# Kernel tuning notes

Measured on AMD Instinct MI355X. Metric: run time of the kernel, lower is better.

The kernel has to match this reference:

```python
import jax, jax.numpy as jnp
import numpy as np

B, C, IMG, P = 8, 6, 384, 16
DIM, HEADS, DEPTH, MLP, NCLS = 768, 12, 4, 3072, 1000
N = (IMG // P) ** 2            # 576 patches
DH = DIM // HEADS              # 64
PATCH_DIM = C * P * P          # 1536


def setup_inputs() -> dict:
    key = jax.random.key(0)
    ks = jax.random.split(key, 13)
    f = lambda k, shp, s=0.02: jax.random.normal(k, shp, jnp.float32) * s
    return {
        "x": jax.random.normal(ks[0], (B, C, IMG, IMG), jnp.float32),
        "patch_w": f(ks[1], (PATCH_DIM, DIM)),
        "patch_b": f(ks[2], (DIM,)),
        "ln1_g": jnp.ones((DEPTH, DIM), jnp.float32),
        "ln1_b": jnp.zeros((DEPTH, DIM), jnp.float32),
        "w_qkv": f(ks[3], (DEPTH, DIM, 3 * DIM)),
        "bias_att": f(ks[4], (DEPTH, HEADS, N, N), 0.5),
        "w_out": f(ks[5], (DEPTH, DIM, DIM)),
        "ln2_g": jnp.ones((DEPTH, DIM), jnp.float32),
        "ln2_b": jnp.zeros((DEPTH, DIM), jnp.float32),
        "w1": f(ks[6], (DEPTH, DIM, MLP)),
        "b1": f(ks[7], (DEPTH, MLP)),
        "w2": f(ks[8], (DEPTH, MLP, DIM)),
        "b2": f(ks[9], (DEPTH, DIM)),
        "lnh_g": jnp.ones((DIM,), jnp.float32),
        "lnh_b": jnp.zeros((DIM,), jnp.float32),
        "w_head": f(ks[10], (DIM, NCLS)),
        "b_head": f(ks[11], (NCLS,)),
    }


def _ln(x, g, b, eps=1e-5):
    m = x.mean(-1, keepdims=True)
    v = ((x - m) ** 2).mean(-1, keepdims=True)
    return (x - m) * jax.lax.rsqrt(v + eps) * g + b


def _patchify(x, patch_w, patch_b):
    # Rearrange 'b c (h p1) (w p2) -> b (h w) (p1 p2 c)' then Linear(patch_dim, dim)
    b = x.shape[0]
    g = IMG // P
    x = x.reshape(b, C, g, P, g, P).transpose(0, 2, 4, 3, 5, 1).reshape(b, g * g, PATCH_DIM)
    return x @ patch_w + patch_b


def _forward(x, patch_w, patch_b, ln1_g, ln1_b, w_qkv, bias_att, w_out,
             ln2_g, ln2_b, w1, b1, w2, b2, lnh_g, lnh_b, w_head, b_head):
    scale = DH ** -0.5
    tok = _patchify(x, patch_w, patch_b)  # [B, N, DIM]; pos_info='mul_att_normed' -> no pos_embed added

    def block(t, p):
        l1g, l1b, wqkv, bias, wout, l2g, l2b, ww1, bb1, ww2, bb2 = p
        h = _ln(t, l1g, l1b)
        qkv = h @ wqkv                                     # [B, N, 3*DIM]
        q, k, v = jnp.split(qkv, 3, axis=-1)
        rs = lambda a: a.reshape(t.shape[0], N, HEADS, DH).transpose(0, 2, 1, 3)
        q, k, v = rs(q), rs(k), rs(v)                      # [B, H, N, DH]
        dots = jnp.einsum('bhid,bhjd->bhij', q, k) * scale
        # mul_att_normed: softmax(qk) * softmax(bias), renormalized over keys
        attn = jax.nn.softmax(dots, axis=-1) * jax.nn.softmax(bias, axis=-1)[None]
        attn = attn / attn.sum(-1, keepdims=True)
        o = jnp.einsum('bhij,bhjd->bhid', attn, v)
        o = o.transpose(0, 2, 1, 3).reshape(t.shape[0], N, DIM) @ wout
        t = t + o
        h2 = _ln(t, l2g, l2b)
        t = t + (jax.nn.gelu(h2 @ ww1 + bb1, approximate=False) @ ww2 + bb2)
        return t, None

    tok, _ = jax.lax.scan(block, tok,
                          (ln1_g, ln1_b, w_qkv, bias_att, w_out,
                           ln2_g, ln2_b, w1, b1, w2, b2))
    pooled = tok.mean(axis=1)                              # mean-pool tokens
    return _ln(pooled, lnh_g, lnh_b) @ w_head + b_head     # [B, NCLS]


def reference(x, patch_w, patch_b, ln1_g, ln1_b, w_qkv, bias_att, w_out,
              ln2_g, ln2_b, w1, b1, w2, b2, lnh_g, lnh_b, w_head, b_head):
    return _forward(x, patch_w, patch_b, ln1_g, ln1_b, w_qkv, bias_att, w_out,
                    ln2_g, ln2_b, w1, b1, w2, b2, lnh_g, lnh_b, w_head, b_head)
```

## Files before the change

kernel.cpp:

```cpp
#include <hip/hip_runtime.h>
#include <hip/hip_bf16.h>

typedef __attribute__((ext_vector_type(8))) short bf16x8;
typedef __attribute__((ext_vector_type(4))) float f32x4;

#define DEVI __device__ __forceinline__

DEVI unsigned short f2bf_bits(float f) {
    __hip_bfloat16 h = __float2bfloat16(f);
    return *reinterpret_cast<unsigned short*>(&h);
}
DEVI float bfbits2f(unsigned short u) {
    __hip_bfloat16 h = *reinterpret_cast<__hip_bfloat16*>(&u);
    return __bfloat162float(h);
}

DEVI void gload_lds16(const void* g, void* lds) {
    __builtin_amdgcn_global_load_lds(
        (const __attribute__((address_space(1))) unsigned int*)g,
        (__attribute__((address_space(3))) unsigned int*)lds, 16, 0, 0);
}

template <int N> DEVI void wait_vm() {
    if constexpr (N == 0) asm volatile("s_waitcnt vmcnt(0)" ::: "memory");
    else if constexpr (N == 4) asm volatile("s_waitcnt vmcnt(4)" ::: "memory");
    else if constexpr (N == 6) asm volatile("s_waitcnt vmcnt(6)" ::: "memory");
    else if constexpr (N == 12) asm volatile("s_waitcnt vmcnt(12)" ::: "memory");
    __builtin_amdgcn_sched_barrier(0);
}
DEVI void lgkm0() {
    asm volatile("s_waitcnt lgkmcnt(0)" ::: "memory");
    __builtin_amdgcn_sched_barrier(0);
}

DEVI int2 remap2d(int bid, int total, int gx) {
    int q = total >> 3, r = total & 7, x = bid & 7, l = bid >> 3;
    int seq = (x < r ? x * (q + 1) : r * (q + 1) + (x - r) * q) + l;
    int g4 = seq / (4 * gx);
    int rem = seq - g4 * 4 * gx;
    return {g4 * 4 + (rem & 3), rem >> 2};
}
DEVI int2 remap2d_g2(int bid, int total, int gx) {
    int q = total >> 3, r = total & 7, x = bid & 7, l = bid >> 3;
    int seq = (x < r ? x * (q + 1) : r * (q + 1) + (x - r) * q) + l;
    int g2 = seq / (2 * gx);
    int rem = seq - g2 * 2 * gx;
    return {g2 * 2 + (rem & 1), rem >> 1};
}

__global__ __launch_bounds__(256) void patchify_kernel(const float* __restrict__ x,
                                                       unsigned short* __restrict__ patches)
{
    size_t t8 = (size_t)blockIdx.x * 256 + threadIdx.x;
    int jq = (int)(t8 % 48);
    size_t t = t8 / 48;
    int r = (int)(t % 384); t /= 384;
    int c = (int)(t % 6);
    int b = (int)(t / 6);
    int j = jq * 8;
    int gh = r >> 4, p1 = r & 15, gw = j >> 4, p2 = j & 15;
    int prow = b * 576 + gh * 24 + gw;
    int pcol = c * 256 + p1 * 16 + p2;
    const float* src = x + ((((size_t)b * 6 + c) * 384 + r) * 384 + j);
    float4 v0 = ((const float4*)src)[0];
    float4 v1 = ((const float4*)src)[1];
    ushort u[8] = { f2bf_bits(v0.x), f2bf_bits(v0.y), f2bf_bits(v0.z), f2bf_bits(v0.w),
                    f2bf_bits(v1.x), f2bf_bits(v1.y), f2bf_bits(v1.z), f2bf_bits(v1.w) };
    *(int4*)&patches[(size_t)prow * 1536 + pcol] = *(int4*)u;
}

__global__ __launch_bounds__(256) void convT_patch_kernel(const float* __restrict__ W,
                                                          __hip_bfloat16* __restrict__ Wt)
{
    __shared__ float tile[32][33];
    int n0 = blockIdx.x * 32, kp0 = blockIdx.y * 32;
    int tx = threadIdx.x & 31, ty = threadIdx.x >> 5;
#pragma unroll
    for (int i = 0; i < 4; i++) {
        int kp = kp0 + ty + 8 * i;
        int k = (kp & 255) * 6 + (kp >> 8);
        tile[ty + 8 * i][tx] = W[(size_t)k * 768 + n0 + tx];
    }
    __syncthreads();
#pragma unroll
    for (int i = 0; i < 4; i++)
        Wt[(size_t)(n0 + ty + 8 * i) * 1536 + kp0 + tx] = __float2bfloat16(tile[tx][ty + 8 * i]);
}

DEVI void convT_body(const float* __restrict__ W, __hip_bfloat16* __restrict__ Wt,
                     int K, int N, int k0, int n0, int tid)
{
    __shared__ float tile[32][33];
    int tx = tid & 31, ty = tid >> 5;
#pragma unroll
    for (int i = 0; i < 4; i++)
        tile[ty + 8 * i][tx] = W[(size_t)(k0 + ty + 8 * i) * N + n0 + tx];
    __syncthreads();
#pragma unroll
    for (int i = 0; i < 4; i++)
        Wt[(size_t)(n0 + ty + 8 * i) * K + k0 + tx] = __float2bfloat16(tile[tx][ty + 8 * i]);
}

__global__ __launch_bounds__(256) void convT4_kernel(const float* __restrict__ wqkv,
                                                     const float* __restrict__ wout,
                                                     const float* __restrict__ w1,
                                                     const float* __restrict__ w2,
                                                     __hip_bfloat16* __restrict__ dst)
{
    int bt = blockIdx.x;
    const float* W; __hip_bfloat16* Wt; int K, N, lt;
    if (bt < 1728)      { W = wqkv; K = 768;  N = 2304; lt = bt;        Wt = dst; }
    else if (bt < 2304) { W = wout; K = 768;  N = 768;  lt = bt - 1728; Wt = dst + 1769472; }
    else if (bt < 4608) { W = w1;   K = 768;  N = 3072; lt = bt - 2304; Wt = dst + 2359296; }
    else                { W = w2;   K = 3072; N = 768;  lt = bt - 4608; Wt = dst + 4718592; }
    int tn = N >> 5;
    convT_body(W, Wt, K, N, (lt / tn) * 32, (lt % tn) * 32, threadIdx.x);
}

DEVI float ld_ln(const float* p) { return *p; }
DEVI float ld_ln(const __hip_bfloat16* p) { return __bfloat162float(*p); }
DEVI void st_ln(float* p, float v) { *p = v; }
DEVI void st_ln(__hip_bfloat16* p, float v) { *p = __float2bfloat16(v); }

template <typename InT, typename OutT>
__global__ __launch_bounds__(256) void ln_kernel(const InT* __restrict__ x,
                                                 const float* __restrict__ g,
                                                 const float* __restrict__ b,
                                                 OutT* __restrict__ out)
{
    int row = blockIdx.x, tid = threadIdx.x;
    const InT* xr = x + (size_t)row * 768;
    float v0 = ld_ln(&xr[tid]), v1 = ld_ln(&xr[tid + 256]), v2 = ld_ln(&xr[tid + 512]);
    float s = v0 + v1 + v2;
    float s2 = v0 * v0 + v1 * v1 + v2 * v2;
#pragma unroll
    for (int m = 32; m >= 1; m >>= 1) { s += __shfl_xor(s, m); s2 += __shfl_xor(s2, m); }
    __shared__ float red[8];
    int w = tid >> 6;
    if ((tid & 63) == 0) { red[w] = s; red[4 + w] = s2; }
    __syncthreads();
    s = red[0] + red[1] + red[2] + red[3];
    s2 = red[4] + red[5] + red[6] + red[7];
    float mean = s * (1.0f / 768.0f);
    float var = s2 * (1.0f / 768.0f) - mean * mean;
    float rstd = rsqrtf(var + 1e-5f);
    OutT* orow = out + (size_t)row * 768;
    st_ln(&orow[tid], (v0 - mean) * rstd * g[tid] + b[tid]);
    st_ln(&orow[tid + 256], (v1 - mean) * rstd * g[tid + 256] + b[tid + 256]);
    st_ln(&orow[tid + 512], (v2 - mean) * rstd * g[tid + 512] + b[tid + 512]);
}

template <bool BIAS, bool GELU>
__global__ __launch_bounds__(512, 2) void gemm_8ph_kernel(
    const __hip_bfloat16* __restrict__ A,
    const __hip_bfloat16* __restrict__ Bt,
    const float* __restrict__ bias,
    __hip_bfloat16* __restrict__ Cb,
    int M, int N, int K, int gx)
{
    __shared__ __align__(16) __hip_bfloat16 AsF[32768];
    __shared__ __align__(16) __hip_bfloat16 BsF[32768];
    const int tid = threadIdx.x;
    const int wid = tid >> 6, lane = tid & 63;
    const int g = lane >> 4, l16 = lane & 15;
    const int wmh = wid >> 2, wnn = wid & 3;

    int2 bc = remap2d_g2(blockIdx.x, gridDim.x, gx);
    const int bm = bc.x * 256, bn = bc.y * 256;

    const int srow = tid >> 2;
    size_t aS[2], bS[2];
#pragma unroll
    for (int i = 0; i < 2; i++) {
        int row = i * 128 + srow;
        int lc = (tid & 3) ^ ((row >> 1) & 3);
        aS[i] = (size_t)(bm + row) * K + lc * 8;
        bS[i] = (size_t)(bn + row) * K + lc * 8;
    }
    auto stageA = [&](int buf, int kh, int tq) {
        const __hip_bfloat16* ap = A + (size_t)tq * 64 + kh * 32;
        __hip_bfloat16* dst = AsF + (buf * 2 + kh) * 8192;
        gload_lds16(ap + aS[0], dst + tid * 8);
        gload_lds16(ap + aS[1], dst + 4096 + tid * 8);
    };
    auto stageB = [&](int buf, int kh, int tq) {
        const __hip_bfloat16* bp = Bt + (size_t)tq * 64 + kh * 32;
        __hip_bfloat16* dst = BsF + (buf * 2 + kh) * 8192;
        gload_lds16(bp + bS[0], dst + tid * 8);
        gload_lds16(bp + bS[1], dst + 4096 + tid * 8);
    };

    const int csw = (l16 >> 1) & 3;
    const int rdo = (g ^ csw) << 3;
    const int aBase = (wmh * 128 + l16) * 32 + rdo;
    const int bBase = (wnn * 64 + l16) * 32 + rdo;

    f32x4 acc[8][4] = {};
    const int nt = K >> 6;

    stageA(0, 0, 0); stageB(0, 0, 0); stageA(0, 1, 0); stageB(0, 1, 0);
    stageA(1, 0, 1); stageB(1, 0, 1);
    wait_vm<4>();
    __builtin_amdgcn_s_barrier();
    __builtin_amdgcn_sched_barrier(0);

    bf16x8 af[8], bf2[2];
    for (int t = 0; t < nt; t++) {
        const int b = t & 1;
        const int k0 = (b * 2 + 0) * 8192, k1 = (b * 2 + 1) * 8192;

#pragma unroll
        for (int mi = 0; mi < 8; mi++) af[mi] = *(const bf16x8*)&AsF[k0 + aBase + mi * 512];
        bf2[0] = *(const bf16x8*)&BsF[k0 + bBase + 0 * 512];
        bf2[1] = *(const bf16x8*)&BsF[k0 + bBase + 1 * 512];
        if (t + 1 < nt) stageA(b ^ 1, 1, t + 1);
        __builtin_amdgcn_s_barrier(); lgkm0();
        __builtin_amdgcn_s_setprio(1);
#pragma unroll
        for (int mi = 0; mi < 8; mi++) {
            acc[mi][0] = __builtin_amdgcn_mfma_f32_16x16x32_bf16(af[mi], bf2[0], acc[mi][0], 0, 0, 0);
            acc[mi][1] = __builtin_amdgcn_mfma_f32_16x16x32_bf16(af[mi], bf2[1], acc[mi][1], 0, 0, 0);
        }
        __builtin_amdgcn_s_setprio(0);
        __builtin_amdgcn_s_barrier();

        bf2[0] = *(const bf16x8*)&BsF[k0 + bBase + 2 * 512];
        bf2[1] = *(const bf16x8*)&BsF[k0 + bBase + 3 * 512];
        if (t + 1 < nt) stageB(b ^ 1, 1, t + 1);
        __builtin_amdgcn_s_barrier(); lgkm0();
        __builtin_amdgcn_s_setprio(1);
#pragma unroll
        for (int mi = 0; mi < 8; mi++) {
            acc[mi][2] = __builtin_amdgcn_mfma_f32_16x16x32_bf16(af[mi], bf2[0], acc[mi][2], 0, 0, 0);
            acc[mi][3] = __builtin_amdgcn_mfma_f32_16x16x32_bf16(af[mi], bf2[1], acc[mi][3], 0, 0, 0);
        }
        __builtin_amdgcn_s_setprio(0);
        __builtin_amdgcn_s_barrier();

#pragma unroll
        for (int mi = 0; mi < 8; mi++) af[mi] = *(const bf16x8*)&AsF[k1 + aBase + mi * 512];
        bf2[0] = *(const bf16x8*)&BsF[k1 + bBase + 0 * 512];
        bf2[1] = *(const bf16x8*)&BsF[k1 + bBase + 1 * 512];
        if (t + 2 < nt) stageA(b, 0, t + 2);
        __builtin_amdgcn_s_barrier(); lgkm0();
        __builtin_amdgcn_s_setprio(1);
#pragma unroll
        for (int mi = 0; mi < 8; mi++) {
            acc[mi][0] = __builtin_amdgcn_mfma_f32_16x16x32_bf16(af[mi], bf2[0], acc[mi][0], 0, 0, 0);
            acc[mi][1] = __builtin_amdgcn_mfma_f32_16x16x32_bf16(af[mi], bf2[1], acc[mi][1], 0, 0, 0);
        }
        __builtin_amdgcn_s_setprio(0);
        __builtin_amdgcn_s_barrier();

        bf2[0] = *(const bf16x8*)&BsF[k1 + bBase + 2 * 512];
        bf2[1] = *(const bf16x8*)&BsF[k1 + bBase + 3 * 512];
        if (t + 2 < nt) stageB(b, 0, t + 2);
        __builtin_amdgcn_s_barrier(); lgkm0();
        __builtin_amdgcn_s_setprio(1);
#pragma unroll
        for (int mi = 0; mi < 8; mi++) {
            acc[mi][2] = __builtin_amdgcn_mfma_f32_16x16x32_bf16(af[mi], bf2[0], acc[mi][2], 0, 0, 0);
            acc[mi][3] = __builtin_amdgcn_mfma_f32_16x16x32_bf16(af[mi], bf2[1], acc[mi][3], 0, 0, 0);
        }
        __builtin_amdgcn_s_setprio(0);
        if (t + 2 < nt) wait_vm<4>();
        else            wait_vm<0>();
        __builtin_amdgcn_s_barrier();
        __builtin_amdgcn_sched_barrier(0);
    }

    __hip_bfloat16* scr = AsF + wid * (16 * 72);
#pragma unroll
    for (int mi = 0; mi < 8; mi++) {
#pragma unroll
        for (int ni = 0; ni < 4; ni++) {
            float bval = 0.0f;
            if (BIAS) bval = bias[bn + wnn * 64 + ni * 16 + l16];
#pragma unroll
            for (int r = 0; r < 4; r++) {
                float v = acc[mi][ni][r] + bval;
                if (GELU) v = 0.5f * v * (1.0f + erff(v * 0.70710678118654752f));
                scr[(4 * g + r) * 72 + ni * 16 + l16] = __float2bfloat16(v);
            }
        }
        lgkm0();
#pragma unroll
        for (int q2 = 0; q2 < 2; q2++) {
            int idx = q2 * 64 + lane;
            int row16 = idx >> 3, ch = idx & 7;
            bf16x8 vv = *(const bf16x8*)&scr[row16 * 72 + ch * 8];
            int grow = bm + wmh * 128 + mi * 16 + row16;
            *(int4*)&Cb[(size_t)grow * N + bn + wnn * 64 + ch * 8] = *(int4*)&vv;
        }
        lgkm0();
    }
}

template <bool BIAS, bool RESID>
__global__ __launch_bounds__(256, 2) void gemm_bt_kernel(
    const __hip_bfloat16* __restrict__ A,
    const __hip_bfloat16* __restrict__ Bt,
    const float* __restrict__ bias,
    const __hip_bfloat16* __restrict__ resid,
    __hip_bfloat16* __restrict__ Cb,
    int M, int N, int K, int gx)
{
    constexpr int BM = 64, SL = 6;
    __shared__ __align__(16) __hip_bfloat16 As[3][BM * 64];
    __shared__ __align__(16) __hip_bfloat16 Bs[3][128 * 64];
    const int tid = threadIdx.x;
    const int wid = tid >> 6, lane = tid & 63;
    const int g = lane >> 4, l16 = lane & 15;
    const int wm = (wid >> 1) * 32, wn = (wid & 1) * 64;

    int2 bc = remap2d(blockIdx.x, gridDim.x, gx);
    const int bm = bc.x * BM, bn = bc.y * 128;

    const int sr32 = tid >> 3, ci = tid & 7;
    const int cg = ci ^ (sr32 & 7);
    const int sdst = tid * 8;
    size_t aOff[2], bOff[4];
#pragma unroll
    for (int i = 0; i < 2; i++) aOff[i] = (size_t)(bm + i * 32 + sr32) * K + cg * 8;
#pragma unroll
    for (int i = 0; i < 4; i++) bOff[i] = (size_t)(bn + i * 32 + sr32) * K + cg * 8;

    auto stage = [&](__hip_bfloat16* asb, __hip_bfloat16* bsb, int tq) {
        const __hip_bfloat16* ap = A + tq * 64;
        const __hip_bfloat16* bp = Bt + tq * 64;
#pragma unroll
        for (int i = 0; i < 2; i++) gload_lds16(ap + aOff[i], asb + i * 2048 + sdst);
#pragma unroll
        for (int i = 0; i < 4; i++) gload_lds16(bp + bOff[i], bsb + i * 2048 + sdst);
    };

    f32x4 acc[2][4] = {};
    const int nt = K >> 6;

    stage(As[0], Bs[0], 0);
    stage(As[1], Bs[1], 1);
    stage(As[2], Bs[2], 2);
    wait_vm<12>();
    __builtin_amdgcn_s_barrier();
    __builtin_amdgcn_sched_barrier(0);

    for (int t = 0; t < nt; t += 3) {
#pragma unroll
        for (int u = 0; u < 3; u++) {
            const int tc = t + u;
            bf16x8 af[2][2], bfr[2][4];
#pragma unroll
            for (int s = 0; s < 2; s++) {
                const int cp = ((s * 4 + g) ^ (l16 & 7)) << 3;
#pragma unroll
                for (int mi = 0; mi < 2; mi++)
                    af[s][mi] = *(const bf16x8*)&As[u][(wm + mi * 16 + l16) * 64 + cp];
#pragma unroll
                for (int ni = 0; ni < 4; ni++)
                    bfr[s][ni] = *(const bf16x8*)&Bs[u][(wn + ni * 16 + l16) * 64 + cp];
            }
#pragma unroll
            for (int s = 0; s < 2; s++)
#pragma unroll
                for (int mi = 0; mi < 2; mi++)
#pragma unroll
                    for (int ni = 0; ni < 4; ni++)
                        acc[mi][ni] = __builtin_amdgcn_mfma_f32_16x16x32_bf16(af[s][mi], bfr[s][ni], acc[mi][ni], 0, 0, 0);

            lgkm0();
            __builtin_amdgcn_s_barrier();
            __builtin_amdgcn_sched_barrier(0);

            if (tc + 3 < nt) stage(As[u], Bs[u], tc + 3);
            if (tc + 1 < nt) {
                if (tc + 4 <= nt)      wait_vm<12>();
                else if (tc + 3 == nt) wait_vm<6>();
                else                   wait_vm<0>();
                __builtin_amdgcn_s_barrier();
                __builtin_amdgcn_sched_barrier(0);
            }
        }
    }

    __hip_bfloat16* scr = &As[0][0] + wid * (16 * 72);
#pragma unroll
    for (int mi = 0; mi < 2; mi++) {
#pragma unroll
        for (int ni = 0; ni < 4; ni++) {
            float bval = 0.0f;
            if (BIAS) bval = bias[bn + wn + ni * 16 + l16];
#pragma unroll
            for (int r = 0; r < 4; r++)
                scr[(4 * g + r) * 72 + ni * 16 + l16] = __float2bfloat16(acc[mi][ni][r] + bval);
        }
        lgkm0();
#pragma unroll
        for (int q2 = 0; q2 < 2; q2++) {
            int row16 = q2 * 8 + (lane >> 3), ch = lane & 7;
            bf16x8 vv = *(const bf16x8*)&scr[row16 * 72 + ch * 8];
            int grow = bm + wm + mi * 16 + row16;
            size_t off = (size_t)grow * N + bn + wn + ch * 8;
            if (RESID) {
                bf16x8 rv = *(const bf16x8*)&resid[off];
#pragma unroll
                for (int e = 0; e < 8; e++)
                    vv[e] = (short)f2bf_bits(bfbits2f((unsigned short)vv[e]) + bfbits2f((unsigned short)rv[e]));
            }
            *(int4*)&Cb[off] = *(int4*)&vv;
        }
        lgkm0();
    }
}

__global__ __launch_bounds__(256) void attn_kernel(const __hip_bfloat16* __restrict__ qkvb,
                                                   const float* __restrict__ bias,
                                                   unsigned short* __restrict__ o)
{
    const int seq = (blockIdx.x & 7) * 108 + (blockIdx.x >> 3);
    const int bb = seq & 7, qt = (seq >> 3) % 9, h = seq / 72;
    const int q0 = qt * 64;
    const int tid = threadIdx.x;
    const int wq = tid >> 6, lane = tid & 63, g = lane >> 4, l16 = lane & 15;

    __shared__ __align__(16) unsigned short Qs[64 * 72];
    __shared__ __align__(16) unsigned short Ks[64 * 72];
    __shared__ __align__(16) unsigned short Vt[64 * 72];
    __shared__ __align__(16) unsigned short Ps[4][16 * 72];

    {
        int r = tid >> 2, cb = (tid & 3) * 16;
        const int4* s4 = (const int4*)&qkvb[(size_t)(bb * 576 + q0 + r) * 2304 + h * 64 + cb];
        int4* d4 = (int4*)&Qs[r * 72 + cb];
        d4[0] = s4[0]; d4[1] = s4[1];
    }
    __syncthreads();
    bf16x8 qf0 = *(const bf16x8*)&Qs[(wq * 16 + l16) * 72 + g * 8];
    bf16x8 qf1 = *(const bf16x8*)&Qs[(wq * 16 + l16) * 72 + 32 + g * 8];

    float m_r[4] = {-1e30f, -1e30f, -1e30f, -1e30f};
    float l_r[4] = {0.f, 0.f, 0.f, 0.f};
    f32x4 oa[4] = {};
    const float* bias_h = bias + (size_t)h * 576 * 576;
    const float scale = 0.125f;

    for (int kt = 0; kt < 576; kt += 64) {
        {
            int r = tid >> 2, cb = (tid & 3) * 16;
            const int4* s4 = (const int4*)&qkvb[(size_t)(bb * 576 + kt + r) * 2304 + 768 + h * 64 + cb];
            int4* d4 = (int4*)&Ks[r * 72 + cb];
            d4[0] = s4[0]; d4[1] = s4[1];
            int key = tid & 63, d0 = (tid >> 6) * 16;
            const unsigned short* vs = (const unsigned short*)&qkvb[(size_t)(bb * 576 + kt + key) * 2304 + 1536 + h * 64 + d0];
            bf16x8 v0 = *(const bf16x8*)vs;
            bf16x8 v1 = *(const bf16x8*)(vs + 8);
#pragma unroll
            for (int e = 0; e < 8; e++) {
                Vt[(d0 + e) * 72 + key] = (unsigned short)v0[e];
                Vt[(d0 + 8 + e) * 72 + key] = (unsigned short)v1[e];
            }
        }
        __syncthreads();

        float bl[4][4];
#pragma unroll
        for (int kc = 0; kc < 4; kc++)
#pragma unroll
            for (int r = 0; r < 4; r++) {
                int q = q0 + wq * 16 + 4 * g + r;
                bl[kc][r] = bias_h[(size_t)q * 576 + kt + kc * 16 + l16];
            }

        f32x4 sc[4] = {};
        __builtin_amdgcn_s_setprio(1);
#pragma unroll
        for (int kc = 0; kc < 4; kc++) {
            bf16x8 kf0 = *(const bf16x8*)&Ks[(kc * 16 + l16) * 72 + g * 8];
            bf16x8 kf1 = *(const bf16x8*)&Ks[(kc * 16 + l16) * 72 + 32 + g * 8];
            sc[kc] = __builtin_amdgcn_mfma_f32_16x16x32_bf16(qf0, kf0, sc[kc], 0, 0, 0);
            sc[kc] = __builtin_amdgcn_mfma_f32_16x16x32_bf16(qf1, kf1, sc[kc], 0, 0, 0);
        }
        __builtin_amdgcn_s_setprio(0);

        float sv[4][4], mt[4] = {-1e30f, -1e30f, -1e30f, -1e30f};
#pragma unroll
        for (int kc = 0; kc < 4; kc++)
#pragma unroll
            for (int r = 0; r < 4; r++) {
                float s = sc[kc][r] * scale + bl[kc][r];
                sv[kc][r] = s;
                mt[r] = fmaxf(mt[r], s);
            }
#pragma unroll
        for (int r = 0; r < 4; r++)
#pragma unroll
            for (int m = 1; m < 16; m <<= 1) mt[r] = fmaxf(mt[r], __shfl_xor(mt[r], m));

        float sf[4];
#pragma unroll
        for (int r = 0; r < 4; r++) {
            float mn = fmaxf(m_r[r], mt[r]);
            sf[r] = __expf(m_r[r] - mn);
            m_r[r] = mn;
        }
        float rs[4] = {0.f, 0.f, 0.f, 0.f};
#pragma unroll
        for (int kc = 0; kc < 4; kc++)
#pragma unroll
            for (int r = 0; r < 4; r++) {
                float p = __expf(sv[kc][r] - m_r[r]);
                rs[r] += p;
                Ps[wq][(4 * g + r) * 72 + kc * 16 + l16] = f2bf_bits(p);
            }
#pragma unroll
        for (int r = 0; r < 4; r++) {
#pragma unroll
            for (int m = 1; m < 16; m <<= 1) rs[r] += __shfl_xor(rs[r], m);
            l_r[r] = l_r[r] * sf[r] + rs[r];
        }
#pragma unroll
        for (int dt = 0; dt < 4; dt++)
#pragma unroll
            for (int r = 0; r < 4; r++) oa[dt][r] *= sf[r];

        asm volatile("s_waitcnt lgkmcnt(0)" ::: "memory");

        __builtin_amdgcn_s_setprio(1);
#pragma unroll
        for (int s = 0; s < 2; s++) {
            bf16x8 pf = *(const bf16x8*)&Ps[wq][l16 * 72 + s * 32 + g * 8];
#pragma unroll
            for (int dt = 0; dt < 4; dt++) {
                bf16x8 vf = *(const bf16x8*)&Vt[(dt * 16 + l16) * 72 + s * 32 + g * 8];
                oa[dt] = __builtin_amdgcn_mfma_f32_16x16x32_bf16(pf, vf, oa[dt], 0, 0, 0);
            }
        }
        __builtin_amdgcn_s_setprio(0);
        __syncthreads();
    }

#pragma unroll
    for (int dt = 0; dt < 4; dt++)
#pragma unroll
        for (int r = 0; r < 4; r++) {
            int q = q0 + wq * 16 + 4 * g + r;
            float v = oa[dt][r] / l_r[r];
            o[(size_t)(bb * 576 + q) * 768 + h * 64 + dt * 16 + l16] = f2bf_bits(v);
        }
}

__global__ __launch_bounds__(256) void pool_kernel(const __hip_bfloat16* __restrict__ tok,
                                                   float* __restrict__ pooled)
{
    int d = blockIdx.x * 256 + threadIdx.x;
    int b = blockIdx.y;
    float s = 0.0f;
    for (int n = 0; n < 576; n++) s += __bfloat162float(tok[(size_t)(b * 576 + n) * 768 + d]);
    pooled[b * 768 + d] = s * (1.0f / 576.0f);
}

__global__ __launch_bounds__(256) void head_kernel(const float* __restrict__ lnp,
                                                   const float* __restrict__ w,
                                                   const float* __restrict__ bh,
                                                   float* __restrict__ out)
{
    int c = blockIdx.x * 256 + threadIdx.x;
    int b = blockIdx.y;
    if (c >= 1000) return;
    float s = bh[c];
    for (int d = 0; d < 768; d++) s += lnp[b * 768 + d] * w[(size_t)d * 1000 + c];
    out[b * 1000 + c] = s;
}

extern "C" void kernel_launch(void* const* d_in, const int* in_sizes, int n_in,
                              void* d_out, int out_size, void* d_ws, size_t ws_size,
                              hipStream_t stream)
{
    const float* x = (const float*)d_in[0];
    const float* patch_w = (const float*)d_in[1];
    const float* patch_b = (const float*)d_in[2];
    const float* ln1_g = (const float*)d_in[3];
    const float* ln1_b = (const float*)d_in[4];
    const float* w_qkv = (const float*)d_in[5];
    const float* bias_att = (const float*)d_in[6];
    const float* w_out = (const float*)d_in[7];
    const float* ln2_g = (const float*)d_in[8];
    const float* ln2_b = (const float*)d_in[9];
    const float* w1 = (const float*)d_in[10];
    const float* b1 = (const float*)d_in[11];
    const float* w2 = (const float*)d_in[12];
    const float* b2 = (const float*)d_in[13];
    const float* lnh_g = (const float*)d_in[14];
    const float* lnh_b = (const float*)d_in[15];
    const float* w_head = (const float*)d_in[16];
    const float* b_head = (const float*)d_in[17];
    float* out = (float*)d_out;

    char* ws = (char*)d_ws;
    __hip_bfloat16* tok = (__hip_bfloat16*)(ws + 0);
    __hip_bfloat16* qkv_bf = (__hip_bfloat16*)(ws + 14155776);
    float* pooled = (float*)(ws + 56623104);
    float* pooledln = (float*)(ws + 56647680);
    __hip_bfloat16* patches = (__hip_bfloat16*)(ws + 56672256);
    __hip_bfloat16* lw = patches;
    __hip_bfloat16* h_bf = (__hip_bfloat16*)(ws + 70828032);
    __hip_bfloat16* o_bf = (__hip_bfloat16*)(ws + 77905920);
    __hip_bfloat16* hid_bf = (__hip_bfloat16*)(ws + 84983808);
    __hip_bfloat16* wbuf = (__hip_bfloat16*)(ws + 113295360);

    patchify_kernel<<<3456, 256, 0, stream>>>(x, (unsigned short*)patches);
    convT_patch_kernel<<<dim3(24, 48), 256, 0, stream>>>(patch_w, wbuf);
    gemm_bt_kernel<true, false><<<432, 256, 0, stream>>>(
        patches, wbuf, patch_b, nullptr, tok, 4608, 768, 1536, 6);

    for (int l = 0; l < 4; l++) {
        convT4_kernel<<<6912, 256, 0, stream>>>(
            w_qkv + (size_t)l * 768 * 2304, w_out + (size_t)l * 768 * 768,
            w1 + (size_t)l * 768 * 3072, w2 + (size_t)l * 3072 * 768, lw);
        ln_kernel<__hip_bfloat16, __hip_bfloat16><<<4608, 256, 0, stream>>>(
            tok, ln1_g + l * 768, ln1_b + l * 768, h_bf);
        gemm_8ph_kernel<false, false><<<162, 512, 0, stream>>>(
            h_bf, lw, nullptr, qkv_bf, 4608, 2304, 768, 9);
        attn_kernel<<<864, 256, 0, stream>>>(
            qkv_bf, bias_att + (size_t)l * 12 * 576 * 576, (unsigned short*)o_bf);
        gemm_bt_kernel<false, true><<<432, 256, 0, stream>>>(
            o_bf, lw + 1769472, nullptr, tok, tok, 4608, 768, 768, 6);
        ln_kernel<__hip_bfloat16, __hip_bfloat16><<<4608, 256, 0, stream>>>(
            tok, ln2_g + l * 768, ln2_b + l * 768, h_bf);
        gemm_8ph_kernel<true, true><<<216, 512, 0, stream>>>(
            h_bf, lw + 2359296, b1 + l * 3072, hid_bf, 4608, 3072, 768, 12);
        gemm_bt_kernel<true, true><<<432, 256, 0, stream>>>(
            hid_bf, lw + 4718592, b2 + l * 768, tok, tok, 4608, 768, 3072, 6);
    }

    pool_kernel<<<dim3(3, 8), 256, 0, stream>>>(tok, pooled);
    ln_kernel<float, float><<<8, 256, 0, stream>>>(pooled, lnh_g, lnh_b, pooledln);
    head_kernel<<<dim3(4, 8), 256, 0, stream>>>(pooledln, w_head, b_head, out);
}
```

Before: 835.7 us.

## Fold LayerNorm into GEMM epilogues via precomputed weight coefficients and row stats

LayerNorm is removed as a separate pass. The gamma scale is folded into the transposed bf16 weights, and per-column sums of beta·W and gamma·W are precomputed. A light stats kernel computes per-row mean and rstd, and the QKV and MLP1 GEMMs apply the normalization in their epilogue while reading the raw token tensor directly. When the workspace is large enough, the weight conversion for all layers runs in one launch before the layer loop. This cuts the h_bf write/read traffic and the per-layer launches, at the cost of numerical differences: the GEMM now runs on unnormalized bf16 tokens with a mean-subtraction correction, and lncoef uses a serial 768-long loop per thread.

```diff
diff --git a/kernel.cpp b/kernel.cpp
--- a/kernel.cpp
+++ b/kernel.cpp
@@ -88,6 +88,7 @@
 }
 
 DEVI void convT_body(const float* __restrict__ W, __hip_bfloat16* __restrict__ Wt,
+                     const float* __restrict__ gvec,
                      int K, int N, int k0, int n0, int tid)
 {
     __shared__ float tile[32][33];
@@ -96,65 +97,138 @@
     for (int i = 0; i < 4; i++)
         tile[ty + 8 * i][tx] = W[(size_t)(k0 + ty + 8 * i) * N + n0 + tx];
     __syncthreads();
+    float gk = gvec ? gvec[k0 + tx] : 1.0f;
 #pragma unroll
     for (int i = 0; i < 4; i++)
-        Wt[(size_t)(n0 + ty + 8 * i) * K + k0 + tx] = __float2bfloat16(tile[tx][ty + 8 * i]);
+        Wt[(size_t)(n0 + ty + 8 * i) * K + k0 + tx] = __float2bfloat16(tile[tx][ty + 8 * i] * gk);
+}
+
+DEVI void convT4_dispatch(int bt, const float* wqkv, const float* wout,
+                          const float* w1, const float* w2,
+                          const float* g1, const float* g2,
+                          __hip_bfloat16* dst, int tid)
+{
+    const float* W; const float* gv = nullptr; __hip_bfloat16* Wt; int K, N, lt;
+    if (bt < 1728)      { W = wqkv; K = 768;  N = 2304; lt = bt;        Wt = dst;           gv = g1; }
+    else if (bt < 2304) { W = wout; K = 768;  N = 768;  lt = bt - 1728; Wt = dst + 1769472; }
+    else if (bt < 4608) { W = w1;   K = 768;  N = 3072; lt = bt - 2304; Wt = dst + 2359296; gv = g2; }
+    else                { W = w2;   K = 3072; N = 768;  lt = bt - 4608; Wt = dst + 4718592; }
+    int tn = N >> 5;
+    convT_body(W, Wt, gv, K, N, (lt / tn) * 32, (lt % tn) * 32, tid);
 }
 
 __global__ __launch_bounds__(256) void convT4_kernel(const float* __restrict__ wqkv,
                                                      const float* __restrict__ wout,
                                                      const float* __restrict__ w1,
                                                      const float* __restrict__ w2,
+                                                     const float* __restrict__ g1,
+                                                     const float* __restrict__ g2,
                                                      __hip_bfloat16* __restrict__ dst)
 {
-    int bt = blockIdx.x;
-    const float* W; __hip_bfloat16* Wt; int K, N, lt;
-    if (bt < 1728)      { W = wqkv; K = 768;  N = 2304; lt = bt;        Wt = dst; }
-    else if (bt < 2304) { W = wout; K = 768;  N = 768;  lt = bt - 1728; Wt = dst + 1769472; }
-    else if (bt < 4608) { W = w1;   K = 768;  N = 3072; lt = bt - 2304; Wt = dst + 2359296; }
-    else                { W = w2;   K = 3072; N = 768;  lt = bt - 4608; Wt = dst + 4718592; }
-    int tn = N >> 5;
-    convT_body(W, Wt, K, N, (lt / tn) * 32, (lt % tn) * 32, threadIdx.x);
-}
-
-DEVI float ld_ln(const float* p) { return *p; }
-DEVI float ld_ln(const __hip_bfloat16* p) { return __bfloat162float(*p); }
-DEVI void st_ln(float* p, float v) { *p = v; }
-DEVI void st_ln(__hip_bfloat16* p, float v) { *p = __float2bfloat16(v); }
-
-template <typename InT, typename OutT>
-__global__ __launch_bounds__(256) void ln_kernel(const InT* __restrict__ x,
-                                                 const float* __restrict__ g,
-                                                 const float* __restrict__ b,
-                                                 OutT* __restrict__ out)
+    convT4_dispatch(blockIdx.x, wqkv, wout, w1, w2, g1, g2, dst, threadIdx.x);
+}
+
+__global__ __launch_bounds__(256) void convT4all_kernel(const float* __restrict__ wqkv,
+                                                        const float* __restrict__ wout,
+                                                        const float* __restrict__ w1,
+                                                        const float* __restrict__ w2,
+                                                        const float* __restrict__ ln1_g,
+                                                        const float* __restrict__ ln2_g,
+                                                        __hip_bfloat16* __restrict__ dst)
+{
+    int l = blockIdx.x / 6912, bt = blockIdx.x % 6912;
+    convT4_dispatch(bt,
+                    wqkv + (size_t)l * 768 * 2304, wout + (size_t)l * 768 * 768,
+                    w1 + (size_t)l * 768 * 3072, w2 + (size_t)l * 3072 * 768,
+                    ln1_g + l * 768, ln2_g + l * 768,
+                    dst + (size_t)l * 7077888, threadIdx.x);
+}
+
+__global__ __launch_bounds__(256) void lncoef_kernel(const float* __restrict__ wqkv,
+                                                     const float* __restrict__ w1,
+                                                     const float* __restrict__ ln1_g,
+                                                     const float* __restrict__ ln1_b,
+                                                     const float* __restrict__ ln2_g,
+                                                     const float* __restrict__ ln2_b,
+                                                     const float* __restrict__ b1,
+                                                     float* __restrict__ coef)
+{
+    int l = blockIdx.y;
+    int n = blockIdx.x * 256 + threadIdx.x;
+    const float* W; const float* g; const float* b; int N; int n0; float* dst; float extra = 0.f;
+    if (n < 2304) { W = wqkv + (size_t)l * 768 * 2304; g = ln1_g + l * 768; b = ln1_b + l * 768;
+                    N = 2304; n0 = n; dst = coef + (size_t)l * 10752; }
+    else          { W = w1 + (size_t)l * 768 * 3072;   g = ln2_g + l * 768; b = ln2_b + l * 768;
+                    N = 3072; n0 = n - 2304; dst = coef + (size_t)l * 10752 + 4608;
+                    extra = b1[l * 3072 + n0]; }
+    float s1 = 0.f, s2 = 0.f;
+    for (int k = 0; k < 768; k++) {
+        float w = W[(size_t)k * N + n0];
+        s1 += b[k] * w;
+        s2 += g[k] * w;
+    }
+    dst[n0] = s1 + extra;
+    dst[(N == 2304 ? 2304 : 3072) + n0] = s2;
+}
+
+__global__ __launch_bounds__(256) void stats_kernel(const __hip_bfloat16* __restrict__ tok,
+                                                    float2* __restrict__ stats)
+{
+    int row = blockIdx.x * 4 + (threadIdx.x >> 6);
+    int lane = threadIdx.x & 63;
+    const unsigned short* tr = (const unsigned short*)(tok + (size_t)row * 768) + lane * 12;
+    float s = 0.f, s2 = 0.f;
+#pragma unroll
+    for (int i = 0; i < 3; i++) {
+        ushort4 u = ((const ushort4*)tr)[i];
+        float v0 = bfbits2f(u.x), v1 = bfbits2f(u.y), v2 = bfbits2f(u.z), v3 = bfbits2f(u.w);
+        s += v0 + v1 + v2 + v3;
+        s2 += v0 * v0 + v1 * v1 + v2 * v2 + v3 * v3;
+    }
+#pragma unroll
+    for (int m = 32; m >= 1; m >>= 1) { s += __shfl_xor(s, m); s2 += __shfl_xor(s2, m); }
+    if (lane == 0) {
+        float mean = s * (1.0f / 768.0f);
+        float var = s2 * (1.0f / 768.0f) - mean * mean;
+        stats[row] = make_float2(mean, rsqrtf(var + 1e-5f));
+    }
+}
+
+__global__ __launch_bounds__(192) void lnf_kernel(const float* __restrict__ x,
+                                                  const float* __restrict__ g,
+                                                  const float* __restrict__ b,
+                                                  float* __restrict__ out)
 {
     int row = blockIdx.x, tid = threadIdx.x;
-    const InT* xr = x + (size_t)row * 768;
-    float v0 = ld_ln(&xr[tid]), v1 = ld_ln(&xr[tid + 256]), v2 = ld_ln(&xr[tid + 512]);
-    float s = v0 + v1 + v2;
-    float s2 = v0 * v0 + v1 * v1 + v2 * v2;
+    float4 v4 = *(const float4*)&x[(size_t)row * 768 + tid * 4];
+    float v[4] = {v4.x, v4.y, v4.z, v4.w};
+    float s = v[0] + v[1] + v[2] + v[3];
+    float s2 = v[0] * v[0] + v[1] * v[1] + v[2] * v[2] + v[3] * v[3];
 #pragma unroll
     for (int m = 32; m >= 1; m >>= 1) { s += __shfl_xor(s, m); s2 += __shfl_xor(s2, m); }
-    __shared__ float red[8];
+    __shared__ float red[6];
     int w = tid >> 6;
-    if ((tid & 63) == 0) { red[w] = s; red[4 + w] = s2; }
+    if ((tid & 63) == 0) { red[w] = s; red[3 + w] = s2; }
     __syncthreads();
-    s = red[0] + red[1] + red[2] + red[3];
-    s2 = red[4] + red[5] + red[6] + red[7];
+    s = red[0] + red[1] + red[2];
+    s2 = red[3] + red[4] + red[5];
     float mean = s * (1.0f / 768.0f);
     float var = s2 * (1.0f / 768.0f) - mean * mean;
     float rstd = rsqrtf(var + 1e-5f);
-    OutT* orow = out + (size_t)row * 768;
-    st_ln(&orow[tid], (v0 - mean) * rstd * g[tid] + b[tid]);
-    st_ln(&orow[tid + 256], (v1 - mean) * rstd * g[tid + 256] + b[tid + 256]);
-    st_ln(&orow[tid + 512], (v2 - mean) * rstd * g[tid + 512] + b[tid + 512]);
-}
-
-template <bool BIAS, bool GELU>
+    float4 g4 = *(const float4*)&g[tid * 4];
+    float4 b4 = *(const float4*)&b[tid * 4];
+    float o[4] = { (v[0] - mean) * rstd * g4.x + b4.x, (v[1] - mean) * rstd * g4.y + b4.y,
+                   (v[2] - mean) * rstd * g4.z + b4.z, (v[3] - mean) * rstd * g4.w + b4.w };
+    *(float4*)&out[(size_t)row * 768 + tid * 4] = make_float4(o[0], o[1], o[2], o[3]);
+}
+
+template <bool GELU>
 __global__ __launch_bounds__(512, 2) void gemm_8ph_kernel(
     const __hip_bfloat16* __restrict__ A,
     const __hip_bfloat16* __restrict__ Bt,
-    const float* __restrict__ bias,
+    const float2* __restrict__ stats,
+    const float* __restrict__ c1v,
+    const float* __restrict__ c2v,
     __hip_bfloat16* __restrict__ Cb,
     int M, int N, int K, int gx)
 {
@@ -272,13 +346,17 @@
     __hip_bfloat16* scr = AsF + wid * (16 * 72);
 #pragma unroll
     for (int mi = 0; mi < 8; mi++) {
+        float2 st[4];
+#pragma unroll
+        for (int r = 0; r < 4; r++)
+            st[r] = stats[bm + wmh * 128 + mi * 16 + 4 * g + r];
 #pragma unroll
         for (int ni = 0; ni < 4; ni++) {
-            float bval = 0.0f;
-            if (BIAS) bval = bias[bn + wnn * 64 + ni * 16 + l16];
+            int gcol = bn + wnn * 64 + ni * 16 + l16;
+            float c1 = c1v[gcol], c2 = c2v[gcol];
 #pragma unroll
             for (int r = 0; r < 4; r++) {
-                float v = acc[mi][ni][r] + bval;
+                float v = st[r].y * (acc[mi][ni][r] - st[r].x * c2) + c1;
                 if (GELU) v = 0.5f * v * (1.0f + erff(v * 0.70710678118654752f));
                 scr[(4 * g + r) * 72 + ni * 16 + l16] = __float2bfloat16(v);
             }
@@ -296,7 +374,7 @@
     }
 }
 
-template <bool BIAS, bool RESID>
+template <bool BIAS, bool RESID, bool GELU>
 __global__ __launch_bounds__(256, 2) void gemm_bt_kernel(
     const __hip_bfloat16* __restrict__ A,
     const __hip_bfloat16* __restrict__ Bt,
@@ -305,7 +383,7 @@
     __hip_bfloat16* __restrict__ Cb,
     int M, int N, int K, int gx)
 {
-    constexpr int BM = 64, SL = 6;
+    constexpr int BM = 64;
     __shared__ __align__(16) __hip_bfloat16 As[3][BM * 64];
     __shared__ __align__(16) __hip_bfloat16 Bs[3][128 * 64];
     const int tid = threadIdx.x;
@@ -390,8 +468,11 @@
             float bval = 0.0f;
             if (BIAS) bval = bias[bn + wn + ni * 16 + l16];
 #pragma unroll
-            for (int r = 0; r < 4; r++)
-                scr[(4 * g + r) * 72 + ni * 16 + l16] = __float2bfloat16(acc[mi][ni][r] + bval);
+            for (int r = 0; r < 4; r++) {
+                float v = acc[mi][ni][r] + bval;
+                if (GELU) v = 0.5f * v * (1.0f + erff(v * 0.70710678118654752f));
+                scr[(4 * g + r) * 72 + ni * 16 + l16] = __float2bfloat16(v);
+            }
         }
         lgkm0();
 #pragma unroll
@@ -598,41 +679,50 @@
     char* ws = (char*)d_ws;
     __hip_bfloat16* tok = (__hip_bfloat16*)(ws + 0);
     __hip_bfloat16* qkv_bf = (__hip_bfloat16*)(ws + 14155776);
+    float* coef = (float*)(ws + 35389440);
+    float2* stats = (float2*)(ws + 35561856);
     float* pooled = (float*)(ws + 56623104);
     float* pooledln = (float*)(ws + 56647680);
     __hip_bfloat16* patches = (__hip_bfloat16*)(ws + 56672256);
     __hip_bfloat16* lw = patches;
-    __hip_bfloat16* h_bf = (__hip_bfloat16*)(ws + 70828032);
     __hip_bfloat16* o_bf = (__hip_bfloat16*)(ws + 77905920);
     __hip_bfloat16* hid_bf = (__hip_bfloat16*)(ws + 84983808);
     __hip_bfloat16* wbuf = (__hip_bfloat16*)(ws + 113295360);
+    __hip_bfloat16* lwAll = (__hip_bfloat16*)(ws + 118013952);
+    const bool useAll = ws_size >= (size_t)118013952 + 56623104;
 
     patchify_kernel<<<3456, 256, 0, stream>>>(x, (unsigned short*)patches);
     convT_patch_kernel<<<dim3(24, 48), 256, 0, stream>>>(patch_w, wbuf);
-    gemm_bt_kernel<true, false><<<432, 256, 0, stream>>>(
+    lncoef_kernel<<<dim3(21, 4), 256, 0, stream>>>(w_qkv, w1, ln1_g, ln1_b, ln2_g, ln2_b, b1, coef);
+    gemm_bt_kernel<true, false, false><<<432, 256, 0, stream>>>(
         patches, wbuf, patch_b, nullptr, tok, 4608, 768, 1536, 6);
 
+    if (useAll)
+        convT4all_kernel<<<27648, 256, 0, stream>>>(w_qkv, w_out, w1, w2, ln1_g, ln2_g, lwAll);
+
     for (int l = 0; l < 4; l++) {
-        convT4_kernel<<<6912, 256, 0, stream>>>(
-            w_qkv + (size_t)l * 768 * 2304, w_out + (size_t)l * 768 * 768,
-            w1 + (size_t)l * 768 * 3072, w2 + (size_t)l * 3072 * 768, lw);
-        ln_kernel<__hip_bfloat16, __hip_bfloat16><<<4608, 256, 0, stream>>>(
-            tok, ln1_g + l * 768, ln1_b + l * 768, h_bf);
-        gemm_8ph_kernel<false, false><<<162, 512, 0, stream>>>(
-            h_bf, lw, nullptr, qkv_bf, 4608, 2304, 768, 9);
+        __hip_bfloat16* lwl = useAll ? lwAll + (size_t)l * 7077888 : lw;
+        const float* cf = coef + (size_t)l * 10752;
+        if (!useAll)
+            convT4_kernel<<<6912, 256, 0, stream>>>(
+                w_qkv + (size_t)l * 768 * 2304, w_out + (size_t)l * 768 * 768,
+                w1 + (size_t)l * 768 * 3072, w2 + (size_t)l * 3072 * 768,
+                ln1_g + l * 768, ln2_g + l * 768, lw);
+        stats_kernel<<<1152, 256, 0, stream>>>(tok, stats);
+        gemm_8ph_kernel<false><<<162, 512, 0, stream>>>(
+            tok, lwl, stats, cf, cf + 2304, qkv_bf, 4608, 2304, 768, 9);
         attn_kernel<<<864, 256, 0, stream>>>(
             qkv_bf, bias_att + (size_t)l * 12 * 576 * 576, (unsigned short*)o_bf);
-        gemm_bt_kernel<false, true><<<432, 256, 0, stream>>>(
-            o_bf, lw + 1769472, nullptr, tok, tok, 4608, 768, 768, 6);
-        ln_kernel<__hip_bfloat16, __hip_bfloat16><<<4608, 256, 0, stream>>>(
-            tok, ln2_g + l * 768, ln2_b + l * 768, h_bf);
-        gemm_8ph_kernel<true, true><<<216, 512, 0, stream>>>(
-            h_bf, lw + 2359296, b1 + l * 3072, hid_bf, 4608, 3072, 768, 12);
-        gemm_bt_kernel<true, true><<<432, 256, 0, stream>>>(
-            hid_bf, lw + 4718592, b2 + l * 768, tok, tok, 4608, 768, 3072, 6);
+        gemm_bt_kernel<false, true, false><<<432, 256, 0, stream>>>(
+            o_bf, lwl + 1769472, nullptr, tok, tok, 4608, 768, 768, 6);
+        stats_kernel<<<1152, 256, 0, stream>>>(tok, stats);
+        gemm_8ph_kernel<true><<<216, 512, 0, stream>>>(
+            tok, lwl + 2359296, stats, cf + 4608, cf + 4608 + 3072, hid_bf, 4608, 3072, 768, 12);
+        gemm_bt_kernel<true, true, false><<<432, 256, 0, stream>>>(
+            hid_bf, lwl + 4718592, b2 + l * 768, tok, tok, 4608, 768, 3072, 6);
     }
 
     pool_kernel<<<dim3(3, 8), 256, 0, stream>>>(tok, pooled);
-    ln_kernel<float, float><<<8, 256, 0, stream>>>(pooled, lnh_g, lnh_b, pooledln);
+    lnf_kernel<<<8, 192, 0, stream>>>(pooled, lnh_g, lnh_b, pooledln);
     head_kernel<<<dim3(4, 8), 256, 0, stream>>>(pooledln, w_head, b_head, out);
 }
```

New measurement: 900.4 us. 7.7% more time.
